# Optimization experiments

Hardware: AMD Instinct MI355X
Metric: run time of the kernel (lower is better)

The kernel has to match this reference:

```python
import jax, jax.numpy as jnp
import numpy as np

DIM = 128; HEADS = 8; WS = 8; SHIFT = 4; B = 8; H = 256; W = 256; T = 1


def _rel_index(ws):
    # faithful port of create_relative_position_index
    coords = np.arange(ws)
    yy, xx = np.meshgrid(coords, coords, indexing='ij')
    cf = np.stack([yy.reshape(-1), xx.reshape(-1)])          # (2, ws*ws)
    rel = cf[:, :, None] - cf[:, None, :]                     # (2, N, N)
    rel[0] += ws - 1
    rel[1] += ws - 1
    return rel[0] * (2 * ws - 1) + rel[1]                     # (N, N) int


def _row_mask(ws, shift):
    jj, ii = np.meshgrid(np.arange(ws), np.arange(ws), indexing='ij')
    return ((jj >= ws - shift) | (ii >= ws - shift)).reshape(-1)  # (N,) bool


def layernorm(x, g, b, eps=1e-5):
    mu = x.mean(-1, keepdims=True)
    var = ((x - mu) ** 2).mean(-1, keepdims=True)
    return (x - mu) * jax.lax.rsqrt(var + eps) * g + b


def setup_inputs() -> dict:
    key = jax.random.key(0)
    ks = jax.random.split(key, 16)
    s = 0.02
    d = DIM
    inp = {
        'x': jax.random.normal(ks[0], (B, T, H, W, d), jnp.float32),
        'wq': jax.random.normal(ks[1], (d, d), jnp.float32) * s,
        'bq': jnp.zeros((d,), jnp.float32),
        'wk': jax.random.normal(ks[2], (d, d), jnp.float32) * s,
        'bk': jnp.zeros((d,), jnp.float32),
        'wv': jax.random.normal(ks[3], (d, d), jnp.float32) * s,
        'bv': jnp.zeros((d,), jnp.float32),
        'wp': jax.random.normal(ks[4], (d, d), jnp.float32) * s,
        'bp': jnp.zeros((d,), jnp.float32),
        'rpb': jax.random.normal(ks[5], (2 * WS - 1, 2 * WS - 1, HEADS), jnp.float32) * s,
        'ln1_g': jnp.ones((d,), jnp.float32),
        'ln1_b': jnp.zeros((d,), jnp.float32),
        'ln2_g': jnp.ones((d,), jnp.float32),
        'ln2_b': jnp.zeros((d,), jnp.float32),
        'w1': jax.random.normal(ks[6], (d, 4 * d), jnp.float32) * s,
        'b1': jnp.zeros((4 * d,), jnp.float32),
        'w2': jax.random.normal(ks[7], (4 * d, d), jnp.float32) * s,
        'b2': jnp.zeros((d,), jnp.float32),
        'gate': jax.random.normal(ks[8], (1, H, W, 1), jnp.float32) * s,
    }
    return inp


def reference(x, wq, bq, wk, bk, wv, bv, wp, bp, rpb, ln1_g, ln1_b, ln2_g, ln2_b, w1, b1, w2, b2, gate):
    Bx, Tx, Hx, Wx, C = x.shape
    skip = x[:, 0]                                             # (B,H,W,C)
    xn = layernorm(x, ln1_g, ln1_b)[:, 0]                      # (B,H,W,C)
    xs = jnp.roll(xn, (-SHIFT, -SHIFT), axis=(1, 2))
    nh, nw, N = Hx // WS, Wx // WS, WS * WS
    # window partition -> (B*nh*nw, N, C)
    xw = xs.reshape(Bx, nh, WS, nw, WS, C).transpose(0, 1, 3, 2, 4, 5).reshape(-1, N, C)
    hd = C // HEADS
    scale = hd ** -0.5
    q = (xw @ wq + bq).reshape(-1, N, HEADS, hd)
    k = (xw @ wk + bk).reshape(-1, N, HEADS, hd)
    v = (xw @ wv + bv).reshape(-1, N, HEADS, hd)
    attn = jnp.einsum('bnhc,bmhc->bnhm', q, k) * scale         # (Bw,N,H,N)
    # relative position bias gather; .view(B,N,heads,N) over (N*N,heads) flat layout
    idx = jnp.asarray(_rel_index(WS).reshape(-1))
    bias = rpb.reshape(-1, HEADS)[idx].reshape(N, HEADS, N)
    attn = attn + bias[None]
    # shift mask: full query rows set to -1e9 (per original patch_mask)
    rmask = jnp.asarray(_row_mask(WS, SHIFT))
    attn = jnp.where(rmask[None, :, None, None], jnp.float32(-1e9), attn)
    attn = jax.nn.softmax(attn, axis=-1)
    out = jnp.einsum('bnhm,bmhc->bnhc', attn, v).reshape(-1, N, C) @ wp + bp
    # window reverse
    xr = out.reshape(Bx, nh, nw, WS, WS, C).transpose(0, 1, 3, 2, 4, 5).reshape(Bx, Hx, Wx, C)
    xa = xs + xr
    xa = jnp.roll(xa, (SHIFT, SHIFT), axis=(1, 2))
    # gated skip
    x2 = xa + jax.nn.sigmoid(gate) * skip
    # MLP (dropout = identity in eval)
    h = jax.nn.gelu(layernorm(x2, ln2_g, ln2_b) @ w1 + b1, approximate=False)
    y = x2 + (h @ w2 + b2)
    return y.reshape(Bx, Tx, Hx, Wx, C)
```

## Files before the change

kernel.cpp:

```cpp
#include <hip/hip_runtime.h>
#include <hip/hip_bf16.h>
#include <math.h>

#define TPB 256

typedef __attribute__((ext_vector_type(8))) __bf16 bf16x8;
typedef __attribute__((ext_vector_type(4))) __bf16 bf16x4;
typedef __attribute__((ext_vector_type(4))) float f32x4;

static __device__ __forceinline__ bf16x8 lds_frag(const char* base, int row, int byteOff, int rowBytes) {
    return *reinterpret_cast<const bf16x8*>(base + row * rowBytes + (byteOff ^ ((row & 7) << 4)));
}
static __device__ __forceinline__ void lds_wr4(char* base, int row, int col0, int rowBytes, f32x4 v) {
    bf16x4 p;
    p[0] = (__bf16)v[0]; p[1] = (__bf16)v[1]; p[2] = (__bf16)v[2]; p[3] = (__bf16)v[3];
    *reinterpret_cast<bf16x4*>(base + row * rowBytes + ((col0 << 1) ^ ((row & 7) << 4))) = p;
}

__global__ void convert_w(const float* __restrict__ wq, const float* __restrict__ wk,
                          const float* __restrict__ wv, const float* __restrict__ wp,
                          const float* __restrict__ w1, const float* __restrict__ w2,
                          const float* __restrict__ rpb, const float* __restrict__ bq,
                          __bf16* __restrict__ ws)
{
    int g = blockIdx.x * 256 + threadIdx.x;
    if (g < 65536) {
        int which = g >> 14, idx = g & 16383, n = idx >> 7, k = idx & 127;
        const float* W = (which == 0) ? wq : (which == 1) ? wk : (which == 2) ? wv : wp;
        float v = W[k * 128 + n];
        if (which == 0) v *= 0.25f;
        ws[g] = (__bf16)v;
    } else if (g < 131072) {
        int idx = g - 65536, n = idx >> 7, k = idx & 127;
        ws[g] = (__bf16)w1[k * 512 + n];
    } else if (g < 196608) {
        int idx = g - 131072, n = idx >> 9, k = idx & 511;
        ws[g] = (__bf16)w2[k * 128 + n];
    } else if (g < 204800) {
        float* wsf = (float*)(ws + 196608);
        int g2 = g - 196608;
        int hc = g2 >> 8, h = hc >> 2, ct = hc & 3;
        int lane = (g2 >> 2) & 63, kg = lane >> 4, ar = lane & 15, r = g2 & 3;
        int dy = (ar >> 2) - h + 7;
        int dx = (ar & 3) - (ct * 2 + (kg >> 1)) + 7;
        int hsrc = ((kg & 1) << 2) | r;
        wsf[g2] = rpb[(dy * 15 + dx) * 8 + hsrc];
    } else if (g < 204928) {
        float* wsf = (float*)(ws + 196608);
        wsf[8192 + (g - 204800)] = bq[g - 204800] * 0.25f;
    }
}

#define O_P     4096
#define O_ATTN  12288
#define O_K     16384
#define O_VT    32768
#define O_Q     49152
#define O_MU    53248
#define O_RS    53504
#define O_GATE  53760
#define O_VMEAN 54016
#define SMEM_SZ 54272

__global__ __launch_bounds__(TPB, 2) void swin_fused_kernel(
    const float* __restrict__ x,
    const __bf16* __restrict__ wqT,
    const __bf16* __restrict__ wkT, const float* __restrict__ bk,
    const __bf16* __restrict__ wvT, const float* __restrict__ bv,
    const __bf16* __restrict__ wpT, const float* __restrict__ bp,
    const float* __restrict__ bias_pre, const float* __restrict__ bqs,
    const float* __restrict__ ln1g, const float* __restrict__ ln1b,
    const float* __restrict__ ln2g, const float* __restrict__ ln2b,
    const __bf16* __restrict__ w1T, const float* __restrict__ b1,
    const __bf16* __restrict__ w2T, const float* __restrict__ b2,
    const float* __restrict__ gate,
    float* __restrict__ out)
{
    __shared__ __align__(16) char smem[SMEM_SZ];
    char* s_xn   = smem;
    char* s_attn = smem + O_ATTN;
    char* s_k    = smem + O_K;
    char* s_vT   = smem + O_VT;
    char* s_xn2  = smem + O_VT;
    char* s_q    = smem + O_Q;
    char* s_h    = smem;
    float* s_proj = (float*)(smem);
    float* s_out  = (float*)(smem);
    float* s_mu   = (float*)(smem + O_MU);
    float* s_rs   = (float*)(smem + O_RS);
    float* s_gate = (float*)(smem + O_GATE);
    __bf16* s_vmean = (__bf16*)(smem + O_VMEAN);

    const int tid = threadIdx.x;
    const int blk = blockIdx.x;
    const int b  = blk >> 10;
    const int wh = (blk >> 5) & 31;
    const int ww = blk & 31;

    const int row = tid >> 2;
    const int l4  = tid & 3;
    float vals[32];

    {
        const int si = wh * 8 + (row >> 3), sj = ww * 8 + (row & 7);
        const int oi = (si + 4) & 255, oj = (sj + 4) & 255;
        const int base = ((b * 256 + oi) * 256 + oj) * 128;
        if (l4 == 0) s_gate[row] = gate[oi * 256 + oj];
        const float* xp = x + base + l4 * 32;
        float sum = 0.f, sq = 0.f;
#pragma unroll
        for (int i = 0; i < 8; ++i) {
            const float4 v4 = reinterpret_cast<const float4*>(xp)[i];
            vals[4*i+0] = v4.x; vals[4*i+1] = v4.y; vals[4*i+2] = v4.z; vals[4*i+3] = v4.w;
            sum += v4.x + v4.y + v4.z + v4.w;
            sq  += v4.x*v4.x + v4.y*v4.y + v4.z*v4.z + v4.w*v4.w;
        }
        sum += __shfl_xor(sum, 1); sum += __shfl_xor(sum, 2);
        sq  += __shfl_xor(sq , 1); sq  += __shfl_xor(sq , 2);
        const float mu  = sum * (1.f / 128.f);
        const float var = sq * (1.f / 128.f) - mu * mu;
        const float rs  = rsqrtf(var + 1e-5f);
        if (l4 == 0) { s_mu[row] = mu; s_rs[row] = rs; }
#pragma unroll
        for (int j = 0; j < 4; ++j) {
            bf16x8 pk;
#pragma unroll
            for (int e = 0; e < 8; ++e) {
                const int d = l4 * 32 + j * 8 + e;
                pk[e] = (__bf16)((vals[j*8+e] - mu) * rs * ln1g[d] + ln1b[d]);
            }
            const int byteOff = (l4 * 64 + j * 16) ^ ((row & 7) << 4);
            *reinterpret_cast<bf16x8*>(s_xn + row * 256 + byteOff) = pk;
        }
    }
    __syncthreads();

    const int lane = tid & 63, w = tid >> 6;
    const int ar = lane & 15, kg = lane >> 4;

    {
        bf16x8 a[4][4];
#pragma unroll
        for (int nt = 0; nt < 4; ++nt)
#pragma unroll
            for (int kc = 0; kc < 4; ++kc)
                a[nt][kc] = lds_frag(s_xn, nt * 16 + ar, kc * 64 + (kg << 4), 256);
        const int nrow = ((ar >> 2) << 3) + (ar & 3);
        bf16x8 aq[4];
#pragma unroll
        for (int kc = 0; kc < 4; ++kc)
            aq[kc] = lds_frag(s_xn, nrow, kc * 64 + (kg << 4), 256);

#pragma unroll
        for (int ct2 = 0; ct2 < 2; ++ct2) {
            const int m0t = (w + ct2 * 4) * 16;
            bf16x8 af[4];
#pragma unroll
            for (int kc = 0; kc < 4; ++kc)
                af[kc] = *reinterpret_cast<const bf16x8*>(wkT + (m0t + ar) * 128 + kc * 32 + (kg << 3));
            const float4 bb4 = *reinterpret_cast<const float4*>(bk + m0t + kg * 4);
#pragma unroll
            for (int nt = 0; nt < 4; ++nt) {
                f32x4 c = {bb4.x, bb4.y, bb4.z, bb4.w};
#pragma unroll
                for (int kc = 0; kc < 4; ++kc)
                    c = __builtin_amdgcn_mfma_f32_16x16x32_bf16(af[kc], a[nt][kc], c, 0, 0, 0);
                lds_wr4(s_k, nt * 16 + ar, m0t + kg * 4, 256, c);
            }
        }
#pragma unroll
        for (int ct2 = 0; ct2 < 2; ++ct2) {
            const int brow = (w + ct2 * 4) * 16 + ar;
            bf16x8 bf[4];
#pragma unroll
            for (int kc = 0; kc < 4; ++kc)
                bf[kc] = *reinterpret_cast<const bf16x8*>(wvT + brow * 128 + kc * 32 + (kg << 3));
            const float bb = bv[brow];
            float vs = 0.f;
#pragma unroll
            for (int rt = 0; rt < 4; ++rt) {
                f32x4 c = {bb, bb, bb, bb};
#pragma unroll
                for (int kc = 0; kc < 4; ++kc)
                    c = __builtin_amdgcn_mfma_f32_16x16x32_bf16(a[rt][kc], bf[kc], c, 0, 0, 0);
                lds_wr4(s_vT, brow, rt * 16 + kg * 4, 128, c);
                vs += c[0] + c[1] + c[2] + c[3];
            }
            vs += __shfl_xor(vs, 16); vs += __shfl_xor(vs, 32);
            if (kg == 0) s_vmean[brow] = (__bf16)(vs * (1.f / 64.f));
        }
#pragma unroll
        for (int ct2 = 0; ct2 < 2; ++ct2) {
            const int m0t = (w + ct2 * 4) * 16;
            bf16x8 af[4];
#pragma unroll
            for (int kc = 0; kc < 4; ++kc)
                af[kc] = *reinterpret_cast<const bf16x8*>(wqT + (m0t + ar) * 128 + kc * 32 + (kg << 3));
            const float4 bb4 = *reinterpret_cast<const float4*>(bqs + m0t + kg * 4);
            f32x4 c = {bb4.x, bb4.y, bb4.z, bb4.w};
#pragma unroll
            for (int kc = 0; kc < 4; ++kc)
                c = __builtin_amdgcn_mfma_f32_16x16x32_bf16(af[kc], aq[kc], c, 0, 0, 0);
            lds_wr4(s_q, ar, m0t + kg * 4, 256, c);
        }
    }
    __syncthreads();

    char* s_p = smem + O_P + (w << 11);
#pragma unroll
    for (int hi = 0; hi < 2; ++hi) {
        const int h = w + hi * 4;
        bf16x8 aQ = {};
        if (lane < 32) aQ = lds_frag(s_q, ar, h * 32 + (kg << 4), 256);
        f32x4 sc[4];
#pragma unroll
        for (int ct = 0; ct < 4; ++ct) {
            bf16x8 bK = {};
            if (lane < 32) bK = lds_frag(s_k, ct * 16 + ar, h * 32 + (kg << 4), 256);
            const f32x4 cin = *reinterpret_cast<const f32x4*>(bias_pre + ((h * 4 + ct) << 8) + (lane << 2));
            sc[ct] = __builtin_amdgcn_mfma_f32_16x16x32_bf16(bK, aQ, cin, 0, 0, 0);
        }
        float sm = 0.f;
#pragma unroll
        for (int ct = 0; ct < 4; ++ct)
#pragma unroll
            for (int r = 0; r < 4; ++r) {
                sc[ct][r] = __expf(sc[ct][r]);
                sm += sc[ct][r];
            }
        sm += __shfl_xor(sm, 16); sm += __shfl_xor(sm, 32);
        const float inv = __builtin_amdgcn_rcpf(sm);
#pragma unroll
        for (int ct = 0; ct < 4; ++ct) {
            f32x4 p4 = {sc[ct][0] * inv, sc[ct][1] * inv, sc[ct][2] * inv, sc[ct][3] * inv};
            lds_wr4(s_p, ar, ct * 16 + kg * 4, 128, p4);
        }
        f32x4 o = {0.f, 0.f, 0.f, 0.f};
#pragma unroll
        for (int kc = 0; kc < 2; ++kc) {
            bf16x8 ap = lds_frag(s_p,  ar, kc * 64 + (kg << 4), 128);
            bf16x8 bV = lds_frag(s_vT, h * 16 + ar, kc * 64 + (kg << 4), 128);
            o = __builtin_amdgcn_mfma_f32_16x16x32_bf16(bV, ap, o, 0, 0, 0);
        }
        lds_wr4(s_attn, ar, h * 16 + kg * 4, 256, o);
    }
    __syncthreads();

    {
        bf16x8 a2[4];
#pragma unroll
        for (int kc = 0; kc < 4; ++kc)
            a2[kc] = lds_frag(s_attn, ar, kc * 64 + (kg << 4), 256);
#pragma unroll
        for (int ct2 = 0; ct2 < 2; ++ct2) {
            const int brow = (w + ct2 * 4) * 16 + ar;
            bf16x8 bf[4];
#pragma unroll
            for (int kc = 0; kc < 4; ++kc)
                bf[kc] = *reinterpret_cast<const bf16x8*>(wpT + brow * 128 + kc * 32 + (kg << 3));
            const float bb = bp[brow];
            f32x4 c = {bb, bb, bb, bb};
#pragma unroll
            for (int kc = 0; kc < 4; ++kc)
                c = __builtin_amdgcn_mfma_f32_16x16x32_bf16(a2[kc], bf[kc], c, 0, 0, 0);
#pragma unroll
            for (int r = 0; r < 4; ++r)
                s_proj[(kg * 4 + r) * 132 + brow] = c[r];
        }
        if (tid < 128) {
            const int col = tid;
            float acc = bp[col];
#pragma unroll
            for (int j = 0; j < 16; ++j) {
                const bf16x8 w8 = *reinterpret_cast<const bf16x8*>(wpT + col * 128 + j * 8);
#pragma unroll
                for (int e = 0; e < 8; ++e)
                    acc += (float)s_vmean[j * 8 + e] * (float)w8[e];
            }
            s_proj[16 * 132 + col] = acc;
        }
    }
    __syncthreads();

    {
        const int si = wh * 8 + (row >> 3), sj = ww * 8 + (row & 7);
        const int oi = (si + 4) & 255, oj = (sj + 4) & 255;
        const int base = ((b * 256 + oi) * 256 + oj) * 128;
        const float sg = 1.f / (1.f + __expf(-s_gate[row]));
        const float mu1 = s_mu[row], rs1 = s_rs[row];
        const bool masked = ((row >> 3) >= 4) || ((row & 7) >= 4);
        const int prow = masked ? 16 : ((row >> 3) * 4 + (row & 7));
        const float* pr = s_proj + prow * 132 + l4 * 32;
        const float* xp = x + base + l4 * 32;
        const float* g1  = ln1g + l4 * 32;
        const float* b1v = ln1b + l4 * 32;
        float sum = 0.f, sq = 0.f;
#pragma unroll
        for (int i = 0; i < 8; ++i) {
            const float4 v4 = reinterpret_cast<const float4*>(xp)[i];
            const float4 gg = reinterpret_cast<const float4*>(g1)[i];
            const float4 bb = reinterpret_cast<const float4*>(b1v)[i];
            const float x4[4] = {v4.x, v4.y, v4.z, v4.w};
            const float g4[4] = {gg.x, gg.y, gg.z, gg.w};
            const float b4[4] = {bb.x, bb.y, bb.z, bb.w};
#pragma unroll
            for (int c = 0; c < 4; ++c) {
                const int idx = 4*i + c;
                const float xv = x4[c];
                const float xnv = (xv - mu1) * rs1 * g4[c] + b4[c];
                const float x2 = xnv + pr[idx] + sg * xv;
                vals[idx] = x2;
                sum += x2; sq += x2 * x2;
            }
        }
        sum += __shfl_xor(sum, 1); sum += __shfl_xor(sum, 2);
        sq  += __shfl_xor(sq , 1); sq  += __shfl_xor(sq , 2);
        const float mu  = sum * (1.f / 128.f);
        const float var = sq * (1.f / 128.f) - mu * mu;
        const float rs  = rsqrtf(var + 1e-5f);
#pragma unroll
        for (int j = 0; j < 4; ++j) {
            bf16x8 pk;
#pragma unroll
            for (int e = 0; e < 8; ++e) {
                const int d = l4 * 32 + j * 8 + e;
                pk[e] = (__bf16)((vals[j*8+e] - mu) * rs * ln2g[d] + ln2b[d]);
            }
            const int byteOff = (l4 * 64 + j * 16) ^ ((row & 7) << 4);
            *reinterpret_cast<bf16x8*>(s_xn2 + row * 256 + byteOff) = pk;
        }
    }
    __syncthreads();

    bf16x8 bx[4][4];
#pragma unroll
    for (int nt = 0; nt < 4; ++nt)
#pragma unroll
        for (int kc = 0; kc < 4; ++kc)
            bx[nt][kc] = lds_frag(s_xn2, nt * 16 + ar, kc * 64 + (kg << 4), 256);

    f32x4 acc2[2][4];
#pragma unroll
    for (int ct2 = 0; ct2 < 2; ++ct2) {
        const float bb = b2[(w + ct2 * 4) * 16 + ar];
#pragma unroll
        for (int rt = 0; rt < 4; ++rt) acc2[ct2][rt] = {bb, bb, bb, bb};
    }

#pragma unroll
    for (int hh = 0; hh < 2; ++hh) {
#pragma unroll
        for (int i = 0; i < 4; ++i) {
            const int hcol0 = (w + 4 * i) * 16;
            const int m0g = hh * 256 + hcol0;
            bf16x8 af[4];
#pragma unroll
            for (int kc = 0; kc < 4; ++kc)
                af[kc] = *reinterpret_cast<const bf16x8*>(w1T + (m0g + ar) * 128 + kc * 32 + (kg << 3));
            const float4 bb4 = *reinterpret_cast<const float4*>(b1 + m0g + kg * 4);
#pragma unroll
            for (int nt = 0; nt < 4; ++nt) {
                f32x4 c = {bb4.x, bb4.y, bb4.z, bb4.w};
#pragma unroll
                for (int kc = 0; kc < 4; ++kc)
                    c = __builtin_amdgcn_mfma_f32_16x16x32_bf16(af[kc], bx[nt][kc], c, 0, 0, 0);
                f32x4 g4;
#pragma unroll
                for (int r = 0; r < 4; ++r) {
                    const float v = c[r];
                    const float u = v * fmaf(0.044715f, v * v, 1.0f);
                    const float e = __expf(-1.5957691216057308f * u);
                    g4[r] = v * __builtin_amdgcn_rcpf(1.0f + e);
                }
                lds_wr4(s_h, nt * 16 + ar, hcol0 + kg * 4, 512, g4);
            }
        }
        __syncthreads();
#pragma unroll
        for (int kc = 0; kc < 8; ++kc) {
            bf16x8 ah[4];
#pragma unroll
            for (int rt = 0; rt < 4; ++rt)
                ah[rt] = lds_frag(s_h, rt * 16 + ar, kc * 64 + (kg << 4), 512);
#pragma unroll
            for (int ct2 = 0; ct2 < 2; ++ct2) {
                const int brow = (w + ct2 * 4) * 16 + ar;
                const bf16x8 bw = *reinterpret_cast<const bf16x8*>(w2T + brow * 512 + hh * 256 + kc * 32 + (kg << 3));
#pragma unroll
                for (int rt = 0; rt < 4; ++rt)
                    acc2[ct2][rt] = __builtin_amdgcn_mfma_f32_16x16x32_bf16(ah[rt], bw, acc2[ct2][rt], 0, 0, 0);
            }
        }
        __syncthreads();
    }

#pragma unroll
    for (int ct2 = 0; ct2 < 2; ++ct2)
#pragma unroll
        for (int rt = 0; rt < 4; ++rt)
#pragma unroll
            for (int r = 0; r < 4; ++r)
                s_out[(rt * 16 + kg * 4 + r) * 132 + (w + ct2 * 4) * 16 + ar] = acc2[ct2][rt][r];
    __syncthreads();
    {
        const int si = wh * 8 + (row >> 3), sj = ww * 8 + (row & 7);
        const int oi = (si + 4) & 255, oj = (sj + 4) & 255;
        const int base = ((b * 256 + oi) * 256 + oj) * 128;
        float* op = out + base + l4 * 32;
        const float* po = s_out + row * 132 + l4 * 32;
#pragma unroll
        for (int i = 0; i < 8; ++i) {
            float4 o;
            o.x = vals[4*i+0] + po[4*i+0];
            o.y = vals[4*i+1] + po[4*i+1];
            o.z = vals[4*i+2] + po[4*i+2];
            o.w = vals[4*i+3] + po[4*i+3];
            reinterpret_cast<float4*>(op)[i] = o;
        }
    }
}

extern "C" void kernel_launch(void* const* d_in, const int* in_sizes, int n_in,
                              void* d_out, int out_size, void* d_ws, size_t ws_size,
                              hipStream_t stream) {
    (void)in_sizes; (void)n_in; (void)ws_size; (void)out_size;
    const float* x    = (const float*)d_in[0];
    const float* wq   = (const float*)d_in[1];
    const float* bq   = (const float*)d_in[2];
    const float* wk   = (const float*)d_in[3];
    const float* bk   = (const float*)d_in[4];
    const float* wv   = (const float*)d_in[5];
    const float* bv   = (const float*)d_in[6];
    const float* wp   = (const float*)d_in[7];
    const float* bp   = (const float*)d_in[8];
    const float* rpb  = (const float*)d_in[9];
    const float* ln1g = (const float*)d_in[10];
    const float* ln1b = (const float*)d_in[11];
    const float* ln2g = (const float*)d_in[12];
    const float* ln2b = (const float*)d_in[13];
    const float* w1   = (const float*)d_in[14];
    const float* b1   = (const float*)d_in[15];
    const float* w2   = (const float*)d_in[16];
    const float* b2   = (const float*)d_in[17];
    const float* gate = (const float*)d_in[18];
    float* out = (float*)d_out;

    __bf16* ws = (__bf16*)d_ws;
    const __bf16* wqT = ws;
    const __bf16* wkT = ws + 16384;
    const __bf16* wvT = ws + 32768;
    const __bf16* wpT = ws + 49152;
    const __bf16* w1T = ws + 65536;
    const __bf16* w2T = ws + 131072;
    const float* wsf  = (const float*)(ws + 196608);
    const float* bias_pre = wsf;
    const float* bqs      = wsf + 8192;

    convert_w<<<801, 256, 0, stream>>>(wq, wk, wv, wp, w1, w2, rpb, bq, ws);
    swin_fused_kernel<<<8192, TPB, 0, stream>>>(x, wqT, wkT, bk, wvT, bv, wpT, bp,
                                                bias_pre, bqs, ln1g, ln1b, ln2g, ln2b,
                                                w1T, b1, w2T, b2, gate, out);
}
```

Baseline: 700.6 us.

## Cut register pressure to fit three blocks per CU

Raises the launch-bounds occupancy target from 2 to 3 blocks per multiprocessor. To make that fit, the K/V projection and the MLP first GEMM now load their activation fragments in halves of 32 rows instead of holding all 64 rows in registers at once, at the cost of reloading weight fragments twice. The residual x re-read from global memory in the post-attention stage is dropped in favour of values already held in registers. The tighter register cap may cause spills, and the extra weight loads add global traffic.

```diff
diff --git a/kernel.cpp b/kernel.cpp
--- a/kernel.cpp
+++ b/kernel.cpp
@@ -62,7 +62,7 @@
 #define O_VMEAN 54016
 #define SMEM_SZ 54272
 
-__global__ __launch_bounds__(TPB, 2) void swin_fused_kernel(
+__global__ __launch_bounds__(TPB, 3) void swin_fused_kernel(
     const float* __restrict__ x,
     const __bf16* __restrict__ wqT,
     const __bf16* __restrict__ wkT, const float* __restrict__ bk,
@@ -139,56 +139,11 @@
     const int ar = lane & 15, kg = lane >> 4;
 
     {
-        bf16x8 a[4][4];
-#pragma unroll
-        for (int nt = 0; nt < 4; ++nt)
-#pragma unroll
-            for (int kc = 0; kc < 4; ++kc)
-                a[nt][kc] = lds_frag(s_xn, nt * 16 + ar, kc * 64 + (kg << 4), 256);
         const int nrow = ((ar >> 2) << 3) + (ar & 3);
         bf16x8 aq[4];
 #pragma unroll
         for (int kc = 0; kc < 4; ++kc)
             aq[kc] = lds_frag(s_xn, nrow, kc * 64 + (kg << 4), 256);
-
-#pragma unroll
-        for (int ct2 = 0; ct2 < 2; ++ct2) {
-            const int m0t = (w + ct2 * 4) * 16;
-            bf16x8 af[4];
-#pragma unroll
-            for (int kc = 0; kc < 4; ++kc)
-                af[kc] = *reinterpret_cast<const bf16x8*>(wkT + (m0t + ar) * 128 + kc * 32 + (kg << 3));
-            const float4 bb4 = *reinterpret_cast<const float4*>(bk + m0t + kg * 4);
-#pragma unroll
-            for (int nt = 0; nt < 4; ++nt) {
-                f32x4 c = {bb4.x, bb4.y, bb4.z, bb4.w};
-#pragma unroll
-                for (int kc = 0; kc < 4; ++kc)
-                    c = __builtin_amdgcn_mfma_f32_16x16x32_bf16(af[kc], a[nt][kc], c, 0, 0, 0);
-                lds_wr4(s_k, nt * 16 + ar, m0t + kg * 4, 256, c);
-            }
-        }
-#pragma unroll
-        for (int ct2 = 0; ct2 < 2; ++ct2) {
-            const int brow = (w + ct2 * 4) * 16 + ar;
-            bf16x8 bf[4];
-#pragma unroll
-            for (int kc = 0; kc < 4; ++kc)
-                bf[kc] = *reinterpret_cast<const bf16x8*>(wvT + brow * 128 + kc * 32 + (kg << 3));
-            const float bb = bv[brow];
-            float vs = 0.f;
-#pragma unroll
-            for (int rt = 0; rt < 4; ++rt) {
-                f32x4 c = {bb, bb, bb, bb};
-#pragma unroll
-                for (int kc = 0; kc < 4; ++kc)
-                    c = __builtin_amdgcn_mfma_f32_16x16x32_bf16(a[rt][kc], bf[kc], c, 0, 0, 0);
-                lds_wr4(s_vT, brow, rt * 16 + kg * 4, 128, c);
-                vs += c[0] + c[1] + c[2] + c[3];
-            }
-            vs += __shfl_xor(vs, 16); vs += __shfl_xor(vs, 32);
-            if (kg == 0) s_vmean[brow] = (__bf16)(vs * (1.f / 64.f));
-        }
 #pragma unroll
         for (int ct2 = 0; ct2 < 2; ++ct2) {
             const int m0t = (w + ct2 * 4) * 16;
@@ -202,6 +157,59 @@
             for (int kc = 0; kc < 4; ++kc)
                 c = __builtin_amdgcn_mfma_f32_16x16x32_bf16(af[kc], aq[kc], c, 0, 0, 0);
             lds_wr4(s_q, ar, m0t + kg * 4, 256, c);
+        }
+
+        float vs[2] = {0.f, 0.f};
+#pragma unroll
+        for (int h2 = 0; h2 < 2; ++h2) {
+            bf16x8 a2[2][4];
+#pragma unroll
+            for (int j = 0; j < 2; ++j)
+#pragma unroll
+                for (int kc = 0; kc < 4; ++kc)
+                    a2[j][kc] = lds_frag(s_xn, (h2 * 2 + j) * 16 + ar, kc * 64 + (kg << 4), 256);
+#pragma unroll
+            for (int ct2 = 0; ct2 < 2; ++ct2) {
+                const int m0t = (w + ct2 * 4) * 16;
+                {
+                    bf16x8 af[4];
+#pragma unroll
+                    for (int kc = 0; kc < 4; ++kc)
+                        af[kc] = *reinterpret_cast<const bf16x8*>(wkT + (m0t + ar) * 128 + kc * 32 + (kg << 3));
+                    const float4 bb4 = *reinterpret_cast<const float4*>(bk + m0t + kg * 4);
+#pragma unroll
+                    for (int j = 0; j < 2; ++j) {
+                        f32x4 c = {bb4.x, bb4.y, bb4.z, bb4.w};
+#pragma unroll
+                        for (int kc = 0; kc < 4; ++kc)
+                            c = __builtin_amdgcn_mfma_f32_16x16x32_bf16(af[kc], a2[j][kc], c, 0, 0, 0);
+                        lds_wr4(s_k, (h2 * 2 + j) * 16 + ar, m0t + kg * 4, 256, c);
+                    }
+                }
+                {
+                    const int brow = m0t + ar;
+                    bf16x8 bf[4];
+#pragma unroll
+                    for (int kc = 0; kc < 4; ++kc)
+                        bf[kc] = *reinterpret_cast<const bf16x8*>(wvT + brow * 128 + kc * 32 + (kg << 3));
+                    const float bbv = bv[brow];
+#pragma unroll
+                    for (int j = 0; j < 2; ++j) {
+                        f32x4 c = {bbv, bbv, bbv, bbv};
+#pragma unroll
+                        for (int kc = 0; kc < 4; ++kc)
+                            c = __builtin_amdgcn_mfma_f32_16x16x32_bf16(a2[j][kc], bf[kc], c, 0, 0, 0);
+                        lds_wr4(s_vT, brow, (h2 * 2 + j) * 16 + kg * 4, 128, c);
+                        vs[ct2] += c[0] + c[1] + c[2] + c[3];
+                    }
+                }
+            }
+        }
+#pragma unroll
+        for (int ct2 = 0; ct2 < 2; ++ct2) {
+            float v = vs[ct2];
+            v += __shfl_xor(v, 16); v += __shfl_xor(v, 32);
+            if (kg == 0) s_vmean[(w + ct2 * 4) * 16 + ar] = (__bf16)(v * (1.f / 64.f));
         }
     }
     __syncthreads();
@@ -283,30 +291,24 @@
     __syncthreads();
 
     {
-        const int si = wh * 8 + (row >> 3), sj = ww * 8 + (row & 7);
-        const int oi = (si + 4) & 255, oj = (sj + 4) & 255;
-        const int base = ((b * 256 + oi) * 256 + oj) * 128;
         const float sg = 1.f / (1.f + __expf(-s_gate[row]));
         const float mu1 = s_mu[row], rs1 = s_rs[row];
         const bool masked = ((row >> 3) >= 4) || ((row & 7) >= 4);
         const int prow = masked ? 16 : ((row >> 3) * 4 + (row & 7));
         const float* pr = s_proj + prow * 132 + l4 * 32;
-        const float* xp = x + base + l4 * 32;
         const float* g1  = ln1g + l4 * 32;
         const float* b1v = ln1b + l4 * 32;
         float sum = 0.f, sq = 0.f;
 #pragma unroll
         for (int i = 0; i < 8; ++i) {
-            const float4 v4 = reinterpret_cast<const float4*>(xp)[i];
             const float4 gg = reinterpret_cast<const float4*>(g1)[i];
             const float4 bb = reinterpret_cast<const float4*>(b1v)[i];
-            const float x4[4] = {v4.x, v4.y, v4.z, v4.w};
             const float g4[4] = {gg.x, gg.y, gg.z, gg.w};
             const float b4[4] = {bb.x, bb.y, bb.z, bb.w};
 #pragma unroll
             for (int c = 0; c < 4; ++c) {
                 const int idx = 4*i + c;
-                const float xv = x4[c];
+                const float xv = vals[idx];
                 const float xnv = (xv - mu1) * rs1 * g4[c] + b4[c];
                 const float x2 = xnv + pr[idx] + sg * xv;
                 vals[idx] = x2;
@@ -332,13 +334,6 @@
     }
     __syncthreads();
 
-    bf16x8 bx[4][4];
-#pragma unroll
-    for (int nt = 0; nt < 4; ++nt)
-#pragma unroll
-        for (int kc = 0; kc < 4; ++kc)
-            bx[nt][kc] = lds_frag(s_xn2, nt * 16 + ar, kc * 64 + (kg << 4), 256);
-
     f32x4 acc2[2][4];
 #pragma unroll
     for (int ct2 = 0; ct2 < 2; ++ct2) {
@@ -350,29 +345,38 @@
 #pragma unroll
     for (int hh = 0; hh < 2; ++hh) {
 #pragma unroll
-        for (int i = 0; i < 4; ++i) {
-            const int hcol0 = (w + 4 * i) * 16;
-            const int m0g = hh * 256 + hcol0;
-            bf16x8 af[4];
-#pragma unroll
-            for (int kc = 0; kc < 4; ++kc)
-                af[kc] = *reinterpret_cast<const bf16x8*>(w1T + (m0g + ar) * 128 + kc * 32 + (kg << 3));
-            const float4 bb4 = *reinterpret_cast<const float4*>(b1 + m0g + kg * 4);
-#pragma unroll
-            for (int nt = 0; nt < 4; ++nt) {
-                f32x4 c = {bb4.x, bb4.y, bb4.z, bb4.w};
+        for (int ntc = 0; ntc < 2; ++ntc) {
+            bf16x8 bx2[2][4];
+#pragma unroll
+            for (int j = 0; j < 2; ++j)
 #pragma unroll
                 for (int kc = 0; kc < 4; ++kc)
-                    c = __builtin_amdgcn_mfma_f32_16x16x32_bf16(af[kc], bx[nt][kc], c, 0, 0, 0);
-                f32x4 g4;
-#pragma unroll
-                for (int r = 0; r < 4; ++r) {
-                    const float v = c[r];
-                    const float u = v * fmaf(0.044715f, v * v, 1.0f);
-                    const float e = __expf(-1.5957691216057308f * u);
-                    g4[r] = v * __builtin_amdgcn_rcpf(1.0f + e);
+                    bx2[j][kc] = lds_frag(s_xn2, (ntc * 2 + j) * 16 + ar, kc * 64 + (kg << 4), 256);
+#pragma unroll
+            for (int i = 0; i < 4; ++i) {
+                const int hcol0 = (w + 4 * i) * 16;
+                const int m0g = hh * 256 + hcol0;
+                bf16x8 af[4];
+#pragma unroll
+                for (int kc = 0; kc < 4; ++kc)
+                    af[kc] = *reinterpret_cast<const bf16x8*>(w1T + (m0g + ar) * 128 + kc * 32 + (kg << 3));
+                const float4 bb4 = *reinterpret_cast<const float4*>(b1 + m0g + kg * 4);
+#pragma unroll
+                for (int j = 0; j < 2; ++j) {
+                    f32x4 c = {bb4.x, bb4.y, bb4.z, bb4.w};
+#pragma unroll
+                    for (int kc = 0; kc < 4; ++kc)
+                        c = __builtin_amdgcn_mfma_f32_16x16x32_bf16(af[kc], bx2[j][kc], c, 0, 0, 0);
+                    f32x4 g4;
+#pragma unroll
+                    for (int r = 0; r < 4; ++r) {
+                        const float v = c[r];
+                        const float u = v * fmaf(0.044715f, v * v, 1.0f);
+                        const float e = __expf(-1.5957691216057308f * u);
+                        g4[r] = v * __builtin_amdgcn_rcpf(1.0f + e);
+                    }
+                    lds_wr4(s_h, (ntc * 2 + j) * 16 + ar, hcol0 + kg * 4, 512, g4);
                 }
-                lds_wr4(s_h, nt * 16 + ar, hcol0 + kg * 4, 512, g4);
             }
         }
         __syncthreads();
```

Measured after the change: 874.9 us. +24.9%, slower.
